# Kernel optimization log

Measured on AMD Instinct MI355X. Metric: run time of the kernel, lower is better.

The kernel has to match this reference:

```python
import jax, jax.numpy as jnp
import numpy as np

B, C_IN, C_OUT, K, H, W_DIM, F_IN = 16, 64, 64, 3, 128, 128, 16
NKW = C_OUT * C_IN * K * K  # 36864 kernel weights per sample


def setup_inputs() -> dict:
    key = jax.random.key(0)
    ks = jax.random.split(key, 8)
    s = 0.05
    return {
        "x": jax.random.normal(ks[0], (B, C_IN, H, W_DIM), dtype=jnp.float32),
        "z": jax.random.normal(ks[1], (B, F_IN), dtype=jnp.float32),
        "W0": jax.random.normal(ks[2], (20, F_IN), dtype=jnp.float32) * s,
        "b0": jax.random.normal(ks[3], (20,), dtype=jnp.float32) * s,
        "W1": jax.random.normal(ks[4], (30, 20), dtype=jnp.float32) * s,
        "b1": jax.random.normal(ks[5], (30,), dtype=jnp.float32) * s,
        "W2": jax.random.normal(ks[6], (NKW + C_OUT, 30), dtype=jnp.float32) * s,
        "b2": jax.random.normal(ks[7], (NKW + C_OUT,), dtype=jnp.float32) * s,
    }


def reference(x, z, W0, b0, W1, b1, W2, b2):
    # Manifold MLP: ReLU after EVERY layer, including the final one (as in original code).
    h = jax.nn.relu(z @ W0.T + b0)
    h = jax.nn.relu(h @ W1.T + b1)
    aw = jax.nn.relu(h @ W2.T + b2)  # [B, NKW + C_OUT]

    kernels = aw[:, :NKW].reshape(B, C_OUT, C_IN, K, K)  # per-sample OIHW kernels
    biases = aw[:, NKW:]  # [B, C_OUT]

    def conv_one(xi, wi, bi):
        # xi: [C_IN, H, W], wi: [C_OUT, C_IN, K, K], bi: [C_OUT]
        y = jax.lax.conv_general_dilated(
            xi[None], wi, window_strides=(1, 1), padding="SAME",
            dimension_numbers=("NCHW", "OIHW", "NCHW"))[0]
        return y + bi[:, None, None]

    out = jax.vmap(conv_one)(x, kernels, biases)  # [B, C_OUT, H, W]
    return jax.nn.relu(out)
```

## Files before the change

kernel.cpp:

```cpp
#include <hip/hip_runtime.h>


typedef __bf16 bf16;
typedef __bf16 bf16x8 __attribute__((ext_vector_type(8)));
typedef float f32x4 __attribute__((ext_vector_type(4)));

#define NB 16
#define CI 64
#define CO 64
#define HH 128
#define WW 128
#define TS 16
#define HALO 18
#define NPL (HALO * HALO)
#define NKW 36864
#define NROWS 36928
#define XHW 130
#define WT2_BYTES ((size_t)NB * 9 * 4096 * 2)
#define BIAS_BYTES 4096
#define XH_BYTES ((size_t)NB * XHW * XHW * CI * 2)
#define WS_NEED (WT2_BYTES + BIAS_BYTES + XH_BYTES)

typedef const __attribute__((address_space(1))) void* gas_ptr;
typedef __attribute__((address_space(3))) void* las_ptr;

__global__ __launch_bounds__(256, 4)
void prep_kernel(const float* __restrict__ x, const float* __restrict__ z,
                 const float* __restrict__ W0, const float* __restrict__ b0,
                 const float* __restrict__ W1, const float* __restrict__ b1,
                 const float* __restrict__ W2, const float* __restrict__ b2,
                 bf16* __restrict__ wt2, float* __restrict__ biases,
                 bf16* __restrict__ xh) {
  const int tid = threadIdx.x;
  if (blockIdx.x < 145) {
    __shared__ float h1s[NB][30];
    if (tid < NB) {
      float h0[20];
      #pragma unroll
      for (int i = 0; i < 20; ++i) {
        float s = b0[i];
        #pragma unroll
        for (int j = 0; j < 16; ++j) s += W0[i * 16 + j] * z[tid * 16 + j];
        h0[i] = fmaxf(s, 0.f);
      }
      #pragma unroll
      for (int i = 0; i < 30; ++i) {
        float s = b1[i];
        #pragma unroll
        for (int j = 0; j < 20; ++j) s += W1[i * 20 + j] * h0[j];
        h1s[tid][i] = fmaxf(s, 0.f);
      }
    }
    __syncthreads();
    const int r = blockIdx.x * 256 + tid;
    if (r >= NROWS) return;
    float w2r[30];
    #pragma unroll
    for (int j = 0; j < 30; ++j) w2r[j] = W2[r * 30 + j];
    const float bb = b2[r];
    const bool isk = r < NKW;
    size_t base = 0;
    if (isk) {
      const int co = r / 576;
      const int rem = r - co * 576;
      const int ci = rem / 9;
      const int tap = rem - ci * 9;
      const int g = co >> 4, mm = co & 15;
      const int kh = ci >> 5, qq = (ci >> 3) & 3, jj = ci & 7;
      base = (size_t)(tap * 8 + g * 2 + kh) * 512 + (size_t)(qq * 16 + mm) * 8 + jj;
    }
    for (int b = 0; b < NB; ++b) {
      float s = bb;
      #pragma unroll
      for (int j = 0; j < 30; ++j) s += w2r[j] * h1s[b][j];
      s = fmaxf(s, 0.f);
      if (isk)
        wt2[(size_t)b * (9 * 4096) + base] = (bf16)s;
      else
        biases[b * CO + (r - NKW)] = s;
    }
    return;
  }

  const int bi = blockIdx.x - 145;
  const int b = bi / 65;
  const int pr = bi - b * 65;
  const int yp0 = pr * 2;

  const int w = tid >> 6, lane = tid & 63;
  const int px0 = w * 32;

  bf16* row0 = xh + ((size_t)(b * XHW + yp0)) * XHW * CI;
  bf16* row1 = row0 + XHW * CI;

  __shared__ __align__(16) bf16 xls[2][128 * 64];

  const bool z0 = (yp0 == 0);
  const bool z1 = (yp0 + 1 == XHW - 1);
  const float* xsrc = x + (((size_t)b * CI + lane) << 14) + px0;

  float v0[32], v1[32];
  if (!z0) {
    const float* s0 = xsrc + ((size_t)(yp0 - 1) << 7);
    #pragma unroll
    for (int j = 0; j < 8; ++j)
      *reinterpret_cast<f32x4*>(&v0[4 * j]) =
          *reinterpret_cast<const f32x4*>(s0 + 4 * j);
  }
  if (!z1) {
    const float* s1 = xsrc + ((size_t)yp0 << 7);
    #pragma unroll
    for (int j = 0; j < 8; ++j)
      *reinterpret_cast<f32x4*>(&v1[4 * j]) =
          *reinterpret_cast<const f32x4*>(s1 + 4 * j);
  }

  const int gq = lane >> 3;
  const int bo = (lane & 7) << 1;
  const bf16x8 zero8 = {};

  if (!z0) {
    #pragma unroll
    for (int p = 0; p < 32; ++p) {
      const int pxl = px0 + p;
      *reinterpret_cast<bf16*>(reinterpret_cast<char*>(xls[0]) + (pxl << 7) +
                               ((gq ^ (pxl & 7)) << 4) + bo) = (bf16)v0[p];
    }
  }
  __syncthreads();
  #pragma unroll
  for (int k = 0; k < 5; ++k) {
    const int it = k * 256 + tid;
    if (it >= XHW * 8) break;
    const int pxp = it >> 3, gr = it & 7;
    bf16x8 vv = zero8;
    if (!z0 && pxp >= 1 && pxp <= 128) {
      const int px = pxp - 1;
      vv = *reinterpret_cast<const bf16x8*>(
          reinterpret_cast<const char*>(xls[0]) + (px << 7) +
          ((gr ^ (px & 7)) << 4));
    }
    *reinterpret_cast<bf16x8*>(row0 + it * 8) = vv;
  }

  if (!z1) {
    #pragma unroll
    for (int p = 0; p < 32; ++p) {
      const int pxl = px0 + p;
      *reinterpret_cast<bf16*>(reinterpret_cast<char*>(xls[1]) + (pxl << 7) +
                               ((gq ^ (pxl & 7)) << 4) + bo) = (bf16)v1[p];
    }
  }
  __syncthreads();
  #pragma unroll
  for (int k = 0; k < 5; ++k) {
    const int it = k * 256 + tid;
    if (it >= XHW * 8) break;
    const int pxp = it >> 3, gr = it & 7;
    bf16x8 vv = zero8;
    if (!z1 && pxp >= 1 && pxp <= 128) {
      const int px = pxp - 1;
      vv = *reinterpret_cast<const bf16x8*>(
          reinterpret_cast<const char*>(xls[1]) + (px << 7) +
          ((gr ^ (px & 7)) << 4));
    }
    *reinterpret_cast<bf16x8*>(row1 + it * 8) = vv;
  }
}

__global__ __launch_bounds__(512, 4)
void conv_kernel(const bf16* __restrict__ xh, const bf16* __restrict__ wt2,
                 const float* __restrict__ bias, float* __restrict__ out) {
  __shared__ __align__(16) bf16 xt[2624 * 8];

  const int id = (blockIdx.x & 7) * 128 + (blockIdx.x >> 3);
  const int b = id >> 6;
  const int x0 = (id & 7) * TS;
  const int y0 = ((id >> 3) & 7) * TS;

  const int tid = threadIdx.x;
  const int lane = tid & 63;
  const int wv = tid >> 6;
  const int m = lane & 15;
  const int q = lane >> 4;

  const char* wbase = (const char*)wt2 + (size_t)b * 73728 + lane * 16;

  bf16x8 abuf[2][4][2];
  #pragma unroll
  for (int i = 0; i < 4; ++i)
    #pragma unroll
    for (int kh = 0; kh < 2; ++kh)
      abuf[0][i][kh] =
          *reinterpret_cast<const bf16x8*>(wbase + (i * 2 + kh) * 1024);

  {
    const char* xb =
        (const char*)xh + (((size_t)(b * XHW + y0)) * XHW + x0) * 128;
    #pragma unroll
    for (int k = 0; k < 5; ++k) {
      const int e = k * 512 + tid;
      const int pl = e >> 3;
      const int gs = (e & 7) ^ (pl & 7);
      const int py = (pl * 57) >> 10;
      const int px = pl - py * 18;
      __builtin_amdgcn_global_load_lds(
          (gas_ptr)(xb + ((py * XHW + px) << 7) + (gs << 4)),
          (las_ptr)((char*)xt + ((k * 512 + wv * 64) << 4)), 16, 0, 0);
    }
    if (wv == 0) {
      const int esrc = min(2560 + lane, 2591);
      const int pl = esrc >> 3;
      const int gs = (esrc & 7) ^ (pl & 7);
      const int py = (pl * 57) >> 10;
      const int px = pl - py * 18;
      __builtin_amdgcn_global_load_lds(
          (gas_ptr)(xb + ((py * XHW + px) << 7) + (gs << 4)),
          (las_ptr)((char*)xt + (2560 << 4)), 16, 0, 0);
    }
  }

  f32x4 acc[4][2];
  #pragma unroll
  for (int i = 0; i < 4; ++i) {
    acc[i][0] = (f32x4){0.f, 0.f, 0.f, 0.f};
    acc[i][1] = (f32x4){0.f, 0.f, 0.f, 0.f};
  }

  const int ty0 = wv * 2;

  __syncthreads();

  #pragma unroll
  for (int tap = 0; tap < 9; ++tap) {
    const int cur = tap & 1, nxt = cur ^ 1;
    if (tap < 8) {
      const char* wt_n = wbase + (tap + 1) * 8192;
      #pragma unroll
      for (int i = 0; i < 4; ++i)
        #pragma unroll
        for (int kh = 0; kh < 2; ++kh)
          abuf[nxt][i][kh] =
              *reinterpret_cast<const bf16x8*>(wt_n + (i * 2 + kh) * 1024);
    }
    const int dy = (tap * 11) >> 5;
    const int dx = tap - dy * 3;
    const int plb = (ty0 + dy) * 18 + dx + m;
    __builtin_amdgcn_s_setprio(1);
    #pragma unroll
    for (int kh = 0; kh < 2; ++kh) {
      const int qk = q + kh * 4;
      #pragma unroll
      for (int j = 0; j < 2; ++j) {
        const int pl = plb + j * 18;
        const bf16x8 bv = *reinterpret_cast<const bf16x8*>(
            reinterpret_cast<const char*>(xt) + (pl << 7) +
            ((qk ^ (pl & 7)) << 4));
        #pragma unroll
        for (int i = 0; i < 4; ++i)
          acc[i][j] = __builtin_amdgcn_mfma_f32_16x16x32_bf16(
              abuf[cur][i][kh], bv, acc[i][j], 0, 0, 0);
      }
    }
    __builtin_amdgcn_s_setprio(0);
  }

  const float* bp = bias + b * CO;
  float* ob = out + ((size_t)(b * CO) << 14) + (size_t)((y0 + ty0) * WW + x0 + m);
  #pragma unroll
  for (int i = 0; i < 4; ++i)
    #pragma unroll
    for (int j = 0; j < 2; ++j)
      #pragma unroll
      for (int r = 0; r < 4; ++r) {
        const int co = i * 16 + q * 4 + r;
        float v = acc[i][j][r] + bp[co];
        ob[((size_t)co << 14) + j * WW] = fmaxf(v, 0.f);
      }
}

__global__ __launch_bounds__(512, 4)
void conv_fb(const float* __restrict__ x, const bf16* __restrict__ wt2,
             const float* __restrict__ bias, float* __restrict__ out) {
  __shared__ __align__(16) bf16 xt[NPL * 64];

  const int id = (blockIdx.x & 7) * 128 + (blockIdx.x >> 3);
  const int b = id >> 6;
  const int x0 = (id & 7) * TS;
  const int y0 = ((id >> 3) & 7) * TS;

  const int tid = threadIdx.x;
  const int lane = tid & 63;
  const int wv = tid >> 6;
  const int m = lane & 15;
  const int q = lane >> 4;

  const char* wbase = (const char*)wt2 + (size_t)b * 73728 + lane * 16;

  bf16x8 abuf[2][4][2];
  #pragma unroll
  for (int i = 0; i < 4; ++i)
    #pragma unroll
    for (int kh = 0; kh < 2; ++kh)
      abuf[0][i][kh] =
          *reinterpret_cast<const bf16x8*>(wbase + (i * 2 + kh) * 1024);

  const float* xb = x + ((size_t)b << 20);
  for (int t = 0; t < 6; ++t) {
    const int it = min(tid + t * 512, NPL * 8 - 1);
    const int cig = ((it >> 2) * 810) >> 16;
    const int pl = it - cig * 324;
    const int py = (pl * 57) >> 10;
    const int px = pl - py * 18;
    int gy = y0 + py - 1, gx = x0 + px - 1;
    const bool inb = ((unsigned)gy < (unsigned)HH) & ((unsigned)gx < (unsigned)WW);
    gy = min(max(gy, 0), HH - 1);
    gx = min(max(gx, 0), WW - 1);
    const float* src = xb + ((size_t)cig << 17) + (gy << 7) + gx;
    bf16x8 v8;
    #pragma unroll
    for (int j = 0; j < 8; ++j)
      v8[j] = inb ? (bf16)src[(size_t)j << 14] : (bf16)0.f;
    if (!(t == 5 && tid >= NPL * 8 - 5 * 512))
      *reinterpret_cast<bf16x8*>(reinterpret_cast<char*>(xt) + (pl << 7) +
                                 ((cig ^ (pl & 7)) << 4)) = v8;
  }

  f32x4 acc[4][2];
  #pragma unroll
  for (int i = 0; i < 4; ++i) {
    acc[i][0] = (f32x4){0.f, 0.f, 0.f, 0.f};
    acc[i][1] = (f32x4){0.f, 0.f, 0.f, 0.f};
  }
  const int ty0 = wv * 2;
  __syncthreads();

  #pragma unroll
  for (int tap = 0; tap < 9; ++tap) {
    const int cur = tap & 1, nxt = cur ^ 1;
    if (tap < 8) {
      const char* wt_n = wbase + (tap + 1) * 8192;
      #pragma unroll
      for (int i = 0; i < 4; ++i)
        #pragma unroll
        for (int kh = 0; kh < 2; ++kh)
          abuf[nxt][i][kh] =
              *reinterpret_cast<const bf16x8*>(wt_n + (i * 2 + kh) * 1024);
    }
    const int dy = (tap * 11) >> 5;
    const int dx = tap - dy * 3;
    const int plb = (ty0 + dy) * 18 + dx + m;
    __builtin_amdgcn_s_setprio(1);
    #pragma unroll
    for (int kh = 0; kh < 2; ++kh) {
      const int qk = q + kh * 4;
      #pragma unroll
      for (int j = 0; j < 2; ++j) {
        const int pl = plb + j * 18;
        const bf16x8 bv = *reinterpret_cast<const bf16x8*>(
            reinterpret_cast<const char*>(xt) + (pl << 7) +
            ((qk ^ (pl & 7)) << 4));
        #pragma unroll
        for (int i = 0; i < 4; ++i)
          acc[i][j] = __builtin_amdgcn_mfma_f32_16x16x32_bf16(
              abuf[cur][i][kh], bv, acc[i][j], 0, 0, 0);
      }
    }
    __builtin_amdgcn_s_setprio(0);
  }

  const float* bp = bias + b * CO;
  float* ob = out + ((size_t)(b * CO) << 14) + (size_t)((y0 + ty0) * WW + x0 + m);
  #pragma unroll
  for (int i = 0; i < 4; ++i)
    #pragma unroll
    for (int j = 0; j < 2; ++j)
      #pragma unroll
      for (int r = 0; r < 4; ++r) {
        const int co = i * 16 + q * 4 + r;
        float v = acc[i][j][r] + bp[co];
        ob[((size_t)co << 14) + j * WW] = fmaxf(v, 0.f);
      }
}

extern "C" void kernel_launch(void* const* d_in, const int* in_sizes, int n_in,
                              void* d_out, int out_size, void* d_ws,
                              size_t ws_size, hipStream_t stream) {
  const float* x = (const float*)d_in[0];
  const float* z = (const float*)d_in[1];
  const float* W0 = (const float*)d_in[2];
  const float* b0 = (const float*)d_in[3];
  const float* W1 = (const float*)d_in[4];
  const float* b1 = (const float*)d_in[5];
  const float* W2 = (const float*)d_in[6];
  const float* b2 = (const float*)d_in[7];
  float* out = (float*)d_out;

  bf16* wt2 = (bf16*)d_ws;
  float* biases = (float*)((char*)d_ws + WT2_BYTES);
  bf16* xh = (bf16*)((char*)d_ws + WT2_BYTES + BIAS_BYTES);

  if (ws_size >= WS_NEED) {
    hipLaunchKernelGGL(prep_kernel, dim3(145 + NB * 65), dim3(256), 0, stream,
                       x, z, W0, b0, W1, b1, W2, b2, wt2, biases, xh);
    hipLaunchKernelGGL(conv_kernel, dim3(1024), dim3(512), 0, stream, xh, wt2,
                       biases, out);
  } else {
    hipLaunchKernelGGL(prep_kernel, dim3(145), dim3(256), 0, stream, x, z, W0,
                       b0, W1, b1, W2, b2, wt2, biases, xh);
    hipLaunchKernelGGL(conv_fb, dim3(1024), dim3(512), 0, stream, x, wt2,
                       biases, out);
  }
}
```

Measured before the change: 159.0 us.

## Give each wave a private halo tile to drop the block barrier

```diff
diff --git a/kernel.cpp b/kernel.cpp
--- a/kernel.cpp
+++ b/kernel.cpp
@@ -171,7 +171,7 @@
 __global__ __launch_bounds__(512, 4)
 void conv_kernel(const bf16* __restrict__ xh, const bf16* __restrict__ wt2,
                  const float* __restrict__ bias, float* __restrict__ out) {
-  __shared__ __align__(16) bf16 xt[2624 * 8];
+  __shared__ __align__(16) bf16 xt[8 * 4608];
 
   const int id = (blockIdx.x & 7) * 128 + (blockIdx.x >> 3);
   const int b = id >> 6;
@@ -195,28 +195,19 @@
           *reinterpret_cast<const bf16x8*>(wbase + (i * 2 + kh) * 1024);
 
   {
-    const char* xb =
-        (const char*)xh + (((size_t)(b * XHW + y0)) * XHW + x0) * 128;
-    #pragma unroll
-    for (int k = 0; k < 5; ++k) {
-      const int e = k * 512 + tid;
+    const char* xb = (const char*)xh +
+                     (((size_t)(b * XHW + (y0 + 2 * wv))) * XHW + x0) * 128;
+    char* ldsb = (char*)xt + wv * 9216;
+    #pragma unroll
+    for (int k = 0; k < 9; ++k) {
+      const int e = k * 64 + lane;
       const int pl = e >> 3;
       const int gs = (e & 7) ^ (pl & 7);
-      const int py = (pl * 57) >> 10;
-      const int px = pl - py * 18;
+      const int lr = (pl * 57) >> 10;
+      const int lx = pl - lr * 18;
       __builtin_amdgcn_global_load_lds(
-          (gas_ptr)(xb + ((py * XHW + px) << 7) + (gs << 4)),
-          (las_ptr)((char*)xt + ((k * 512 + wv * 64) << 4)), 16, 0, 0);
-    }
-    if (wv == 0) {
-      const int esrc = min(2560 + lane, 2591);
-      const int pl = esrc >> 3;
-      const int gs = (esrc & 7) ^ (pl & 7);
-      const int py = (pl * 57) >> 10;
-      const int px = pl - py * 18;
-      __builtin_amdgcn_global_load_lds(
-          (gas_ptr)(xb + ((py * XHW + px) << 7) + (gs << 4)),
-          (las_ptr)((char*)xt + (2560 << 4)), 16, 0, 0);
+          (gas_ptr)(xb + ((lr * XHW + lx) << 7) + (gs << 4)),
+          (las_ptr)(ldsb + k * 1024), 16, 0, 0);
     }
   }
 
@@ -227,9 +218,10 @@
     acc[i][1] = (f32x4){0.f, 0.f, 0.f, 0.f};
   }
 
-  const int ty0 = wv * 2;
-
-  __syncthreads();
+  asm volatile("s_waitcnt vmcnt(0)" ::: "memory");
+  __builtin_amdgcn_sched_barrier(0);
+
+  const char* wxt = (const char*)xt + wv * 9216;
 
   #pragma unroll
   for (int tap = 0; tap < 9; ++tap) {
@@ -245,7 +237,7 @@
     }
     const int dy = (tap * 11) >> 5;
     const int dx = tap - dy * 3;
-    const int plb = (ty0 + dy) * 18 + dx + m;
+    const int plb = dy * 18 + dx + m;
     __builtin_amdgcn_s_setprio(1);
     #pragma unroll
     for (int kh = 0; kh < 2; ++kh) {
@@ -254,8 +246,7 @@
       for (int j = 0; j < 2; ++j) {
         const int pl = plb + j * 18;
         const bf16x8 bv = *reinterpret_cast<const bf16x8*>(
-            reinterpret_cast<const char*>(xt) + (pl << 7) +
-            ((qk ^ (pl & 7)) << 4));
+            wxt + (pl << 7) + ((qk ^ (pl & 7)) << 4));
         #pragma unroll
         for (int i = 0; i < 4; ++i)
           acc[i][j] = __builtin_amdgcn_mfma_f32_16x16x32_bf16(
@@ -266,7 +257,8 @@
   }
 
   const float* bp = bias + b * CO;
-  float* ob = out + ((size_t)(b * CO) << 14) + (size_t)((y0 + ty0) * WW + x0 + m);
+  float* ob =
+      out + ((size_t)(b * CO) << 14) + (size_t)((y0 + 2 * wv) * WW + x0 + m);
   #pragma unroll
   for (int i = 0; i < 4; ++i)
     #pragma unroll
```

Result: slower. 165.0 us (+3.7%).

## Split prep into separate hypernetwork and half-row transpose kernels

Applied to the files above, without the earlier changes.

```diff
diff --git a/kernel.cpp b/kernel.cpp
--- a/kernel.cpp
+++ b/kernel.cpp
@@ -24,93 +24,96 @@
 typedef const __attribute__((address_space(1))) void* gas_ptr;
 typedef __attribute__((address_space(3))) void* las_ptr;
 
-__global__ __launch_bounds__(256, 4)
-void prep_kernel(const float* __restrict__ x, const float* __restrict__ z,
-                 const float* __restrict__ W0, const float* __restrict__ b0,
-                 const float* __restrict__ W1, const float* __restrict__ b1,
-                 const float* __restrict__ W2, const float* __restrict__ b2,
-                 bf16* __restrict__ wt2, float* __restrict__ biases,
-                 bf16* __restrict__ xh) {
+__global__ __launch_bounds__(256)
+void hyper_kernel(const float* __restrict__ z, const float* __restrict__ W0,
+                  const float* __restrict__ b0, const float* __restrict__ W1,
+                  const float* __restrict__ b1, const float* __restrict__ W2,
+                  const float* __restrict__ b2, bf16* __restrict__ wt2,
+                  float* __restrict__ biases) {
+  __shared__ float h1s[NB][30];
   const int tid = threadIdx.x;
-  if (blockIdx.x < 145) {
-    __shared__ float h1s[NB][30];
-    if (tid < NB) {
-      float h0[20];
-      #pragma unroll
-      for (int i = 0; i < 20; ++i) {
-        float s = b0[i];
-        #pragma unroll
-        for (int j = 0; j < 16; ++j) s += W0[i * 16 + j] * z[tid * 16 + j];
-        h0[i] = fmaxf(s, 0.f);
-      }
-      #pragma unroll
-      for (int i = 0; i < 30; ++i) {
-        float s = b1[i];
-        #pragma unroll
-        for (int j = 0; j < 20; ++j) s += W1[i * 20 + j] * h0[j];
-        h1s[tid][i] = fmaxf(s, 0.f);
-      }
-    }
-    __syncthreads();
-    const int r = blockIdx.x * 256 + tid;
-    if (r >= NROWS) return;
-    float w2r[30];
-    #pragma unroll
-    for (int j = 0; j < 30; ++j) w2r[j] = W2[r * 30 + j];
-    const float bb = b2[r];
-    const bool isk = r < NKW;
-    size_t base = 0;
-    if (isk) {
-      const int co = r / 576;
-      const int rem = r - co * 576;
-      const int ci = rem / 9;
-      const int tap = rem - ci * 9;
-      const int g = co >> 4, mm = co & 15;
-      const int kh = ci >> 5, qq = (ci >> 3) & 3, jj = ci & 7;
-      base = (size_t)(tap * 8 + g * 2 + kh) * 512 + (size_t)(qq * 16 + mm) * 8 + jj;
-    }
-    for (int b = 0; b < NB; ++b) {
-      float s = bb;
-      #pragma unroll
-      for (int j = 0; j < 30; ++j) s += w2r[j] * h1s[b][j];
-      s = fmaxf(s, 0.f);
-      if (isk)
-        wt2[(size_t)b * (9 * 4096) + base] = (bf16)s;
-      else
-        biases[b * CO + (r - NKW)] = s;
-    }
-    return;
-  }
-
-  const int bi = blockIdx.x - 145;
-  const int b = bi / 65;
-  const int pr = bi - b * 65;
+  if (tid < NB) {
+    float h0[20];
+    #pragma unroll
+    for (int i = 0; i < 20; ++i) {
+      float s = b0[i];
+      #pragma unroll
+      for (int j = 0; j < 16; ++j) s += W0[i * 16 + j] * z[tid * 16 + j];
+      h0[i] = fmaxf(s, 0.f);
+    }
+    #pragma unroll
+    for (int i = 0; i < 30; ++i) {
+      float s = b1[i];
+      #pragma unroll
+      for (int j = 0; j < 20; ++j) s += W1[i * 20 + j] * h0[j];
+      h1s[tid][i] = fmaxf(s, 0.f);
+    }
+  }
+  __syncthreads();
+  const int r = blockIdx.x * 256 + tid;
+  if (r >= NROWS) return;
+  float w2r[30];
+  #pragma unroll
+  for (int j = 0; j < 30; ++j) w2r[j] = W2[r * 30 + j];
+  const float bb = b2[r];
+  const bool isk = r < NKW;
+  size_t base = 0;
+  if (isk) {
+    const int co = r / 576;
+    const int rem = r - co * 576;
+    const int ci = rem / 9;
+    const int tap = rem - ci * 9;
+    const int g = co >> 4, mm = co & 15;
+    const int kh = ci >> 5, qq = (ci >> 3) & 3, jj = ci & 7;
+    base = (size_t)(tap * 8 + g * 2 + kh) * 512 + (size_t)(qq * 16 + mm) * 8 + jj;
+  }
+  for (int b = 0; b < NB; ++b) {
+    float s = bb;
+    #pragma unroll
+    for (int j = 0; j < 30; ++j) s += w2r[j] * h1s[b][j];
+    s = fmaxf(s, 0.f);
+    if (isk)
+      wt2[(size_t)b * (9 * 4096) + base] = (bf16)s;
+    else
+      biases[b * CO + (r - NKW)] = s;
+  }
+}
+
+__global__ __launch_bounds__(256, 8)
+void xpose_kernel(const float* __restrict__ x, bf16* __restrict__ xh) {
+  const int tid = threadIdx.x;
+  const int bi = blockIdx.x;
+  const int b = bi / 130;
+  const int rem = bi - b * 130;
+  const int pr = rem >> 1;
+  const int h = rem & 1;
   const int yp0 = pr * 2;
 
-  const int w = tid >> 6, lane = tid & 63;
-  const int px0 = w * 32;
+  const int lane = tid & 63;
+  const int w = tid >> 6;
+  const int px0 = h * 64 + w * 16;
 
   bf16* row0 = xh + ((size_t)(b * XHW + yp0)) * XHW * CI;
   bf16* row1 = row0 + XHW * CI;
 
-  __shared__ __align__(16) bf16 xls[2][128 * 64];
+  __shared__ __align__(16) bf16 xls[2][64 * 64];
 
   const bool z0 = (yp0 == 0);
   const bool z1 = (yp0 + 1 == XHW - 1);
   const float* xsrc = x + (((size_t)b * CI + lane) << 14) + px0;
 
-  float v0[32], v1[32];
+  float v0[16], v1[16];
   if (!z0) {
     const float* s0 = xsrc + ((size_t)(yp0 - 1) << 7);
     #pragma unroll
-    for (int j = 0; j < 8; ++j)
+    for (int j = 0; j < 4; ++j)
       *reinterpret_cast<f32x4*>(&v0[4 * j]) =
           *reinterpret_cast<const f32x4*>(s0 + 4 * j);
   }
   if (!z1) {
     const float* s1 = xsrc + ((size_t)yp0 << 7);
     #pragma unroll
-    for (int j = 0; j < 8; ++j)
+    for (int j = 0; j < 4; ++j)
       *reinterpret_cast<f32x4*>(&v1[4 * j]) =
           *reinterpret_cast<const f32x4*>(s1 + 4 * j);
   }
@@ -121,50 +124,52 @@
 
   if (!z0) {
     #pragma unroll
-    for (int p = 0; p < 32; ++p) {
-      const int pxl = px0 + p;
+    for (int p = 0; p < 16; ++p) {
+      const int pxl = w * 16 + p;
       *reinterpret_cast<bf16*>(reinterpret_cast<char*>(xls[0]) + (pxl << 7) +
                                ((gq ^ (pxl & 7)) << 4) + bo) = (bf16)v0[p];
     }
   }
   __syncthreads();
   #pragma unroll
-  for (int k = 0; k < 5; ++k) {
+  for (int k = 0; k < 3; ++k) {
     const int it = k * 256 + tid;
-    if (it >= XHW * 8) break;
-    const int pxp = it >> 3, gr = it & 7;
+    if (it >= 65 * 8) break;
+    const int pxp = h * 65 + (it >> 3);
+    const int gr = it & 7;
     bf16x8 vv = zero8;
     if (!z0 && pxp >= 1 && pxp <= 128) {
-      const int px = pxp - 1;
+      const int pxl = pxp - 1 - h * 64;
       vv = *reinterpret_cast<const bf16x8*>(
-          reinterpret_cast<const char*>(xls[0]) + (px << 7) +
-          ((gr ^ (px & 7)) << 4));
-    }
-    *reinterpret_cast<bf16x8*>(row0 + it * 8) = vv;
+          reinterpret_cast<const char*>(xls[0]) + (pxl << 7) +
+          ((gr ^ (pxl & 7)) << 4));
+    }
+    *reinterpret_cast<bf16x8*>(row0 + h * 4160 + it * 8) = vv;
   }
 
   if (!z1) {
     #pragma unroll
-    for (int p = 0; p < 32; ++p) {
-      const int pxl = px0 + p;
+    for (int p = 0; p < 16; ++p) {
+      const int pxl = w * 16 + p;
       *reinterpret_cast<bf16*>(reinterpret_cast<char*>(xls[1]) + (pxl << 7) +
                                ((gq ^ (pxl & 7)) << 4) + bo) = (bf16)v1[p];
     }
   }
   __syncthreads();
   #pragma unroll
-  for (int k = 0; k < 5; ++k) {
+  for (int k = 0; k < 3; ++k) {
     const int it = k * 256 + tid;
-    if (it >= XHW * 8) break;
-    const int pxp = it >> 3, gr = it & 7;
+    if (it >= 65 * 8) break;
+    const int pxp = h * 65 + (it >> 3);
+    const int gr = it & 7;
     bf16x8 vv = zero8;
     if (!z1 && pxp >= 1 && pxp <= 128) {
-      const int px = pxp - 1;
+      const int pxl = pxp - 1 - h * 64;
       vv = *reinterpret_cast<const bf16x8*>(
-          reinterpret_cast<const char*>(xls[1]) + (px << 7) +
-          ((gr ^ (px & 7)) << 4));
-    }
-    *reinterpret_cast<bf16x8*>(row1 + it * 8) = vv;
+          reinterpret_cast<const char*>(xls[1]) + (pxl << 7) +
+          ((gr ^ (pxl & 7)) << 4));
+    }
+    *reinterpret_cast<bf16x8*>(row1 + h * 4160 + it * 8) = vv;
   }
 }
 
@@ -400,14 +405,14 @@
   float* biases = (float*)((char*)d_ws + WT2_BYTES);
   bf16* xh = (bf16*)((char*)d_ws + WT2_BYTES + BIAS_BYTES);
 
+  hipLaunchKernelGGL(hyper_kernel, dim3((NROWS + 255) / 256), dim3(256), 0,
+                     stream, z, W0, b0, W1, b1, W2, b2, wt2, biases);
   if (ws_size >= WS_NEED) {
-    hipLaunchKernelGGL(prep_kernel, dim3(145 + NB * 65), dim3(256), 0, stream,
-                       x, z, W0, b0, W1, b1, W2, b2, wt2, biases, xh);
+    hipLaunchKernelGGL(xpose_kernel, dim3(NB * 65 * 2), dim3(256), 0, stream,
+                       x, xh);
     hipLaunchKernelGGL(conv_kernel, dim3(1024), dim3(512), 0, stream, xh, wt2,
                        biases, out);
   } else {
-    hipLaunchKernelGGL(prep_kernel, dim3(145), dim3(256), 0, stream, x, z, W0,
-                       b0, W1, b1, W2, b2, wt2, biases, xh);
     hipLaunchKernelGGL(conv_fb, dim3(1024), dim3(512), 0, stream, x, wt2,
                        biases, out);
   }
```

Measured after the change: 176.3 us. 10.9% more time.
